# Optimization experiments

Hardware: AMD Instinct MI355X
Metric: run time of the kernel (lower is better)

The kernel has to match this reference:

```python
import jax, jax.numpy as jnp
import numpy as np
import math

B, L, E, H, FF = 8, 1024, 1024, 16, 4096
DH = E // H  # 64
EPS = 1e-10


def layer_norm(x, gamma, beta):
    mean = jnp.mean(x, axis=-1, keepdims=True)
    var = jnp.mean((x - mean) ** 2, axis=-1, keepdims=True)
    return gamma * (x - mean) / jnp.sqrt(var + EPS) + beta


def setup_inputs() -> dict:
    key = jax.random.key(0)
    ks = jax.random.split(key, 16)
    c_qk = math.sqrt(6.0 / (E + DH))
    c_o = math.sqrt(6.0 / (H * DH + E))
    c1 = math.sqrt(6.0 / (E + FF))
    c2 = math.sqrt(6.0 / (FF + E))
    u = lambda k, shp, c: jax.random.uniform(k, shp, jnp.float32, -c, c)
    return {
        "x": jax.random.normal(ks[0], (B, L, E), jnp.float32),
        # per-head projections stacked: [H, E, DH] (stored input-major = W^T of torch Linear)
        "Wq": u(ks[1], (H, E, DH), c_qk), "bq": jnp.zeros((H, DH), jnp.float32),
        "Wk": u(ks[2], (H, E, DH), c_qk), "bk": jnp.zeros((H, DH), jnp.float32),
        "Wv": u(ks[3], (H, E, DH), c_qk), "bv": jnp.zeros((H, DH), jnp.float32),
        "Wo": u(ks[4], (H * DH, E), c_o), "bo": jnp.zeros((E,), jnp.float32),
        "W1": u(ks[5], (E, FF), c1), "b1": jnp.zeros((FF,), jnp.float32),
        "W2": u(ks[6], (FF, E), c2), "b2": jnp.zeros((E,), jnp.float32),
        "gamma1": jnp.ones((E,), jnp.float32), "beta1": jnp.zeros((E,), jnp.float32),
        "gamma2": jnp.ones((E,), jnp.float32), "beta2": jnp.zeros((E,), jnp.float32),
    }


def reference(x, Wq, bq, Wk, bk, Wv, bv, Wo, bo, W1, b1, W2, b2, gamma1, beta1, gamma2, beta2):
    # multi-head attention (all heads batched; concat order == head order)
    q = jnp.einsum("ble,hed->bhld", x, Wq) + bq[None, :, None, :]
    k = jnp.einsum("ble,hed->bhld", x, Wk) + bk[None, :, None, :]
    v = jnp.einsum("ble,hed->bhld", x, Wv) + bv[None, :, None, :]
    scores = jnp.einsum("bhld,bhmd->bhlm", q, k) / math.sqrt(DH)
    weights = jax.nn.softmax(scores, axis=-1)
    y = jnp.einsum("bhlm,bhmd->bhld", weights, v)          # [B,H,L,DH]
    concat = y.transpose(0, 2, 1, 3).reshape(B, L, H * DH)  # [B,L,E]
    out1 = concat @ Wo + bo
    # residual + LN (dropout p=0 -> identity)
    out2 = layer_norm(out1 + x, gamma1, beta1)
    # FFN
    out3 = jax.nn.relu(out2 @ W1 + b1) @ W2 + b2
    return layer_norm(out3 + out2, gamma2, beta2)
```

## Files before the change

### kernel.cpp

```cpp
#include <hip/hip_runtime.h>
#include <hip/hip_bf16.h>

#define BB 8
#define LL 1024
#define EE 1024
#define HH 16
#define DHH 64
#define FFF 4096

typedef __attribute__((ext_vector_type(8))) short short8;
typedef __attribute__((ext_vector_type(4))) float f32x4;

__device__ inline f32x4 mfma16(short8 a, short8 b, f32x4 c) {
    return __builtin_amdgcn_mfma_f32_16x16x32_bf16(a, b, c, 0, 0, 0);
}

__device__ inline void async_ld16(const __hip_bfloat16* g, __hip_bfloat16* l) {
    __builtin_amdgcn_global_load_lds(
        (const __attribute__((address_space(1))) void*)g,
        (__attribute__((address_space(3))) void*)l, 16, 0, 0);
}

__device__ inline unsigned short bf16bits(float f) {
    __hip_bfloat16 h = __float2bfloat16(f);
    return *reinterpret_cast<unsigned short*>(&h);
}

__device__ inline float bf2f(unsigned short u) {
    unsigned v = ((unsigned)u) << 16;
    return *reinterpret_cast<float*>(&v);
}

__device__ inline float exp2_fast(float x) {
    float r;
    asm("v_exp_f32 %0, %1" : "=v"(r) : "v"(x));
    return r;
}

__device__ inline unsigned cvt_pk_bf16(float lo, float hi) {
    unsigned r;
    asm("v_cvt_pk_bf16_f32 %0, %1, %2" : "=v"(r) : "v"(lo), "v"(hi));
    return r;
}

__device__ inline void wg_barrier() {
    __builtin_amdgcn_sched_barrier(0);
    asm volatile("" ::: "memory");
    __builtin_amdgcn_s_barrier();
    asm volatile("" ::: "memory");
    __builtin_amdgcn_sched_barrier(0);
}

__global__ __launch_bounds__(256) void cvt_bf16(const float* __restrict__ in,
                                                __hip_bfloat16* __restrict__ out) {
    size_t i = (size_t)blockIdx.x * 256 + threadIdx.x;
    float4 v = reinterpret_cast<const float4*>(in)[i];
    ushort4 o;
    o.x = bf16bits(v.x); o.y = bf16bits(v.y); o.z = bf16bits(v.z); o.w = bf16bits(v.w);
    reinterpret_cast<ushort4*>(out)[i] = o;
}

__global__ __launch_bounds__(256) void wtrans_all(
    const float* __restrict__ Wq, const float* __restrict__ Wk, const float* __restrict__ Wv,
    const float* __restrict__ Wo, const float* __restrict__ W1, const float* __restrict__ W2,
    __hip_bfloat16* __restrict__ wqkvt, __hip_bfloat16* __restrict__ wot,
    __hip_bfloat16* __restrict__ w1t, __hip_bfloat16* __restrict__ w2t) {
    const int id = blockIdx.x;
    const float* src;
    __hip_bfloat16* dst;
    int K, N, k0, n0;
    if (id < 768) {
        const int which = id >> 8, r = id & 255;
        const int z = r >> 4, xx = r & 15;
        src = ((which == 0) ? Wq : (which == 1) ? Wk : Wv) + (size_t)z * 65536;
        dst = wqkvt + (size_t)which * 1024 * 1024 + (size_t)z * 65536;
        K = 1024; N = 64; k0 = xx * 64; n0 = 0;
    } else if (id < 1024) {
        const int r = id - 768;
        src = Wo; dst = wot; K = 1024; N = 1024; k0 = (r & 15) * 64; n0 = (r >> 4) * 64;
    } else if (id < 2048) {
        const int r = id - 1024;
        src = W1; dst = w1t; K = 1024; N = 4096; k0 = (r & 15) * 64; n0 = (r >> 4) * 64;
    } else {
        const int r = id - 2048;
        src = W2; dst = w2t; K = 4096; N = 1024; k0 = (r & 63) * 64; n0 = (r >> 6) * 64;
    }
    __shared__ __hip_bfloat16 t[64 * 66];
    const int tid = threadIdx.x;
#pragma unroll
    for (int i = 0; i < 16; ++i) {
        int idx = tid + i * 256;
        int kr = idx >> 6, nc = idx & 63;
        t[kr * 66 + nc] = __float2bfloat16(src[(size_t)(k0 + kr) * N + n0 + nc]);
    }
    __syncthreads();
#pragma unroll
    for (int i = 0; i < 16; ++i) {
        int idx = tid + i * 256;
        int nr = idx >> 6, kc = idx & 63;
        dst[(size_t)(n0 + nr) * K + k0 + kc] = t[kc * 66 + nr];
    }
}

__global__ __launch_bounds__(256) void vtrans(const __hip_bfloat16* __restrict__ qkv,
                                              __hip_bfloat16* __restrict__ vt) {
    const int bh = blockIdx.x, lt = blockIdx.y;
    const int b = bh >> 4, h = bh & 15;
    __shared__ __hip_bfloat16 t[64 * 66];
    const int tid = threadIdx.x;
#pragma unroll
    for (int i = 0; i < 16; ++i) {
        int idx = tid + i * 256;
        int lr = idx >> 6, d = idx & 63;
        t[lr * 66 + d] = qkv[(size_t)(b * LL + lt * 64 + lr) * 3072 + 2048 + h * 64 + d];
    }
    __syncthreads();
#pragma unroll
    for (int i = 0; i < 16; ++i) {
        int idx = tid + i * 256;
        int dr = idx >> 6, lc = idx & 63;
        vt[((size_t)bh * 64 + dr) * LL + lt * 64 + lc] = t[lc * 66 + dr];
    }
}

template <int MODE, int CM, int CN, int ZX>
__global__ __launch_bounds__(512, 2) void gemm256(
    const __hip_bfloat16* __restrict__ A, const __hip_bfloat16* __restrict__ Bm,
    int M, int N, int K, int ksplit, size_t zstride, void* __restrict__ Cout,
    const float* __restrict__ bias0, const float* __restrict__ bias1,
    const float* __restrict__ bias2) {
    __shared__ __hip_bfloat16 lds[2][2][2][128 * 64];
    const int flat = blockIdx.x + gridDim.x * (blockIdx.y + gridDim.y * blockIdx.z);
    const int xcd = flat & 7, rank = flat >> 3;
    const int mc = xcd & 3, hc = xcd >> 2;
    const int ml = rank / CN, nl = rank % CN;
    const int mb = mc * CM + ml;
    const int nb = ZX ? nl : (hc * CN + nl);
    const int zb = ZX ? hc : 0;
    const int m0 = mb * 256, n0 = nb * 256;
    const int tid = threadIdx.x;
    const int wid = tid >> 6, l = tid & 63;
    const int wm = wid >> 2, wn = wid & 3;
    const int lr = l & 15, lg = l >> 4;
    const int T = K / (64 * ksplit);
    const int kb = zb * T;

    const int c0 = tid, c1 = tid + 512;
    const int r0 = c0 >> 3, s0 = (((c0 & 7) ^ (r0 & 7)) << 3);
    const int r1 = c1 >> 3, s1 = (((c1 & 7) ^ (r1 & 7)) << 3);
    const int ldst0 = wid * 512;
    const int ldst1 = 4096 + wid * 512;

#define STAGE(bi, isb, half, kt)                                                             \
    do {                                                                                     \
        const __hip_bfloat16* _s = (isb) ? Bm : A;                                           \
        const int _br = ((isb) ? n0 : m0) + (half) * 128;                                    \
        __hip_bfloat16* _d = &lds[bi][isb][half][0];                                         \
        async_ld16(_s + (size_t)(_br + r0) * K + (size_t)(kb + (kt)) * 64 + s0, _d + ldst0); \
        async_ld16(_s + (size_t)(_br + r1) * K + (size_t)(kb + (kt)) * 64 + s1, _d + ldst1); \
    } while (0)

    f32x4 acc[8][4];
#pragma unroll
    for (int m = 0; m < 8; ++m)
#pragma unroll
        for (int n = 0; n < 4; ++n) acc[m][n] = (f32x4){0.f, 0.f, 0.f, 0.f};

    short8 aLo[4][2], aHi[4][2], bR[4][2];

#define LDA(dst, bi, m, kh)                                                          \
    do {                                                                             \
        const int _ra = (m) * 16 + lr;                                               \
        const int _sl = ((kh) * 4 + lg) ^ (_ra & 7);                                 \
        dst = *reinterpret_cast<const short8*>(&lds[bi][0][wm][_ra * 64 + _sl * 8]); \
    } while (0)
#define LDB(dst, bi, n, kh)                                                               \
    do {                                                                                  \
        const int _rb = (wn & 1) * 64 + (n) * 16 + lr;                                    \
        const int _sl = ((kh) * 4 + lg) ^ (_rb & 7);                                      \
        dst = *reinterpret_cast<const short8*>(&lds[bi][1][wn >> 1][_rb * 64 + _sl * 8]); \
    } while (0)

#define RD_ALO(bi)                      \
    _Pragma("unroll") for (int m = 0; m < 4; ++m) { \
        LDA(aLo[m][0], bi, m, 0);       \
        LDA(aLo[m][1], bi, m, 1);       \
    }
#define RD_AHI(bi)                      \
    _Pragma("unroll") for (int m = 0; m < 4; ++m) { \
        LDA(aHi[m][0], bi, m + 4, 0);   \
        LDA(aHi[m][1], bi, m + 4, 1);   \
    }
#define RD_B01(bi)                      \
    _Pragma("unroll") for (int n = 0; n < 2; ++n) { \
        LDB(bR[n][0], bi, n, 0);        \
        LDB(bR[n][1], bi, n, 1);        \
    }
#define RD_B23(bi)                      \
    _Pragma("unroll") for (int n = 2; n < 4; ++n) { \
        LDB(bR[n][0], bi, n, 0);        \
        LDB(bR[n][1], bi, n, 1);        \
    }
#define MFMA_Q(mbase, afr, nlo)                                            \
    __builtin_amdgcn_s_setprio(1);                                         \
    _Pragma("unroll") for (int m = 0; m < 4; ++m) {                        \
        _Pragma("unroll") for (int n = (nlo); n < (nlo) + 2; ++n) {        \
            acc[(mbase) + m][n] = mfma16(afr[m][0], bR[n][0], acc[(mbase) + m][n]); \
            acc[(mbase) + m][n] = mfma16(afr[m][1], bR[n][1], acc[(mbase) + m][n]); \
        }                                                                  \
    }                                                                      \
    __builtin_amdgcn_s_setprio(0);

    STAGE(0, 1, 0, 0);
    STAGE(0, 1, 1, 0);
    STAGE(0, 0, 0, 0);
    STAGE(0, 0, 1, 0);
    if (T > 1) {
        STAGE(1, 1, 0, 1);
        STAGE(1, 1, 1, 1);
        STAGE(1, 0, 0, 1);
        asm volatile("s_waitcnt vmcnt(6)" ::: "memory");
    } else {
        asm volatile("s_waitcnt vmcnt(0)" ::: "memory");
    }
    wg_barrier();
    RD_ALO(0);
    RD_B01(0);

    for (int t = 0; t < T; ++t) {
        const int cur = t & 1, nxt = cur ^ 1;
        wg_barrier();
        MFMA_Q(0, aLo, 0);
        RD_B23(cur);
        if (t + 1 < T) STAGE(nxt, 0, 1, t + 1);
        wg_barrier();
        MFMA_Q(0, aLo, 2);
        RD_AHI(cur);
        if (t + 2 < T) STAGE(cur, 1, 0, t + 2);
        wg_barrier();
        MFMA_Q(4, aHi, 0);
        if (t + 2 < T) {
            asm volatile("s_waitcnt vmcnt(2)" ::: "memory");
            STAGE(cur, 1, 1, t + 2);
            STAGE(cur, 0, 0, t + 2);
        } else if (t + 1 < T) {
            asm volatile("s_waitcnt vmcnt(0)" ::: "memory");
        }
        wg_barrier();
        MFMA_Q(4, aHi, 2);
        if (t + 1 < T) {
            RD_ALO(nxt);
            RD_B01(nxt);
        }
    }
#undef STAGE
#undef LDA
#undef LDB
#undef RD_ALO
#undef RD_AHI
#undef RD_B01
#undef RD_B23
#undef MFMA_Q

    asm volatile("s_waitcnt vmcnt(0)" ::: "memory");
    __syncthreads();

    float* eb = reinterpret_cast<float*>(&lds[0][0][0][0]) + wid * (16 * 68);
    const int erow = l >> 3, ec = l & 7;
    const int rowg = m0 + wm * 128;
    const int colg = n0 + wn * 64;
    float bv[4];
#pragma unroll
    for (int n = 0; n < 4; ++n) {
        if constexpr (MODE == 0) {
            const int col = colg + n * 16 + lr;
            int s = col >> 10;
            const float* bp = (s == 0) ? bias0 : ((s == 1) ? bias1 : bias2);
            bv[n] = bp[col & 1023];
        } else if constexpr (MODE == 2) {
            bv[n] = bias0[colg + n * 16 + lr];
        } else {
            bv[n] = 0.f;
        }
    }
    __hip_bfloat16* Cb = (MODE == 4)
        ? ((__hip_bfloat16*)Cout + (size_t)zb * zstride)
        : (__hip_bfloat16*)Cout;
#pragma unroll
    for (int m = 0; m < 8; ++m) {
#pragma unroll
        for (int n = 0; n < 4; ++n)
#pragma unroll
            for (int r = 0; r < 4; ++r) {
                float v = acc[m][n][r] + bv[n];
                if constexpr (MODE == 2) v = fmaxf(v, 0.f);
                eb[(lg * 4 + r) * 68 + n * 16 + lr] = v;
            }
#pragma unroll
        for (int i = 0; i < 2; ++i) {
            const int rr = erow + i * 8;
            float4 v0 = *reinterpret_cast<float4*>(&eb[rr * 68 + ec * 8]);
            float4 v1 = *reinterpret_cast<float4*>(&eb[rr * 68 + ec * 8 + 4]);
            uint4 o;
            o.x = cvt_pk_bf16(v0.x, v0.y);
            o.y = cvt_pk_bf16(v0.z, v0.w);
            o.z = cvt_pk_bf16(v1.x, v1.y);
            o.w = cvt_pk_bf16(v1.z, v1.w);
            *reinterpret_cast<uint4*>(&Cb[(size_t)(rowg + m * 16 + rr) * N + colg + ec * 8]) = o;
        }
    }
}

__global__ __launch_bounds__(512) void attn3(const __hip_bfloat16* __restrict__ qkv,
                                             const __hip_bfloat16* __restrict__ vt,
                                             __hip_bfloat16* __restrict__ cat) {
    const int orig = blockIdx.y * 8 + blockIdx.x;
    const int swz = (orig & 7) * 128 + (orig >> 3);
    const int qt = swz & 7, bh = swz >> 3;
    const int b = bh >> 4, h = bh & 15;
    const int tid = threadIdx.x, w = tid >> 6, l = tid & 63;
    const int lr = l & 15, lg = l >> 4;
    const int sw = lr & 7;

    __shared__ __hip_bfloat16 Ks[2][64 * 64];
    __shared__ __hip_bfloat16 Vs[2][64 * 64];
    __shared__ __hip_bfloat16 plds[8][16 * 72];

    const size_t qrow = (size_t)(b * LL + qt * 128 + w * 16 + lr);
    const short8 qa0 = *reinterpret_cast<const short8*>(qkv + qrow * 3072 + h * 64 + lg * 8);
    const short8 qa1 = *reinterpret_cast<const short8*>(qkv + qrow * 3072 + h * 64 + 32 + lg * 8);

    const int rA = tid >> 3, sA = (((tid & 7) ^ (rA & 7)) << 3);
    const __hip_bfloat16* kg = qkv + (size_t)(b * LL + rA) * 3072 + 1024 + h * 64 + sA;
    const __hip_bfloat16* vg = vt + ((size_t)bh * 64 + rA) * LL + sA;

#define STAGE_KV(bi, k0)                                        \
    do {                                                        \
        async_ld16(kg + (size_t)(k0) * 3072, &Ks[bi][w * 512]); \
        async_ld16(vg + (k0), &Vs[bi][w * 512]);                \
    } while (0)

    float mrun = -INFINITY, lrun = 0.f;
    f32x4 oacc[4];
#pragma unroll
    for (int n = 0; n < 4; ++n) oacc[n] = (f32x4){0.f, 0.f, 0.f, 0.f};

    STAGE_KV(0, 0);
    asm volatile("s_waitcnt vmcnt(0)" ::: "memory");
    __syncthreads();

    const float SCALE = 0.18033688011112042f;

    int cur = 0;
    for (int kt = 0; kt < 16; ++kt) {
        if (kt < 15) STAGE_KV(cur ^ 1, (kt + 1) * 64);

        f32x4 s[4];
#pragma unroll
        for (int m = 0; m < 4; ++m) {
            const int krow = m * 16 + lr;
            const short8 kf0 =
                *reinterpret_cast<const short8*>(&Ks[cur][krow * 64 + ((lg ^ sw) << 3)]);
            const short8 kf1 =
                *reinterpret_cast<const short8*>(&Ks[cur][krow * 64 + (((lg + 4) ^ sw) << 3)]);
            f32x4 t = (f32x4){0.f, 0.f, 0.f, 0.f};
            t = mfma16(kf0, qa0, t);
            t = mfma16(kf1, qa1, t);
            s[m] = t * SCALE;
        }
        float smax = s[0][0];
#pragma unroll
        for (int m = 0; m < 4; ++m)
#pragma unroll
            for (int r = 0; r < 4; ++r) smax = fmaxf(smax, s[m][r]);
        smax = fmaxf(smax, __shfl_xor(smax, 16, 64));
        smax = fmaxf(smax, __shfl_xor(smax, 32, 64));
        if (__any(smax > mrun + 8.0f)) {
            const float mnew = fmaxf(mrun, smax);
            const float alpha = exp2_fast(mrun - mnew);
            mrun = mnew;
            lrun *= alpha;
#pragma unroll
            for (int r = 0; r < 4; ++r) {
                const float aD = __shfl(alpha, lg * 4 + r, 64);
#pragma unroll
                for (int n = 0; n < 4; ++n) oacc[n][r] *= aD;
            }
        }
        float p[4][4];
        float tsum = 0.f;
#pragma unroll
        for (int m = 0; m < 4; ++m)
#pragma unroll
            for (int r = 0; r < 4; ++r) {
                p[m][r] = exp2_fast(s[m][r] - mrun);
                tsum += p[m][r];
            }
        tsum += __shfl_xor(tsum, 16, 64);
        tsum += __shfl_xor(tsum, 32, 64);
        lrun += tsum;

#pragma unroll
        for (int m = 0; m < 4; ++m) {
            uint2 d;
            d.x = cvt_pk_bf16(p[m][0], p[m][1]);
            d.y = cvt_pk_bf16(p[m][2], p[m][3]);
            *reinterpret_cast<uint2*>(&plds[w][lr * 72 + m * 16 + lg * 4]) = d;
        }
        asm volatile("s_waitcnt lgkmcnt(0)" ::: "memory");
        __builtin_amdgcn_sched_barrier(0);

        const short8 pa0 = *reinterpret_cast<const short8*>(&plds[w][lr * 72 + lg * 8]);
        const short8 pa1 = *reinterpret_cast<const short8*>(&plds[w][lr * 72 + 32 + lg * 8]);
#pragma unroll
        for (int n = 0; n < 4; ++n) {
            const int vrow = n * 16 + lr;
            const short8 vf0 =
                *reinterpret_cast<const short8*>(&Vs[cur][vrow * 64 + ((lg ^ sw) << 3)]);
            const short8 vf1 =
                *reinterpret_cast<const short8*>(&Vs[cur][vrow * 64 + (((lg + 4) ^ sw) << 3)]);
            oacc[n] = mfma16(pa0, vf0, oacc[n]);
            oacc[n] = mfma16(pa1, vf1, oacc[n]);
        }

        asm volatile("s_waitcnt vmcnt(0)" ::: "memory");
        __syncthreads();
        cur ^= 1;
    }
#undef STAGE_KV

    float rinv[4];
#pragma unroll
    for (int r = 0; r < 4; ++r) rinv[r] = 1.0f / __shfl(lrun, lg * 4 + r, 64);
#pragma unroll
    for (int n = 0; n < 4; ++n)
#pragma unroll
        for (int r = 0; r < 4; ++r) {
            const float v = oacc[n][r] * rinv[r];
            cat[(size_t)(b * LL + qt * 128 + w * 16 + lg * 4 + r) * EE + h * 64 + n * 16 + lr] =
                __float2bfloat16(v);
        }
}

template <bool CBF16, bool OUTF32>
__global__ __launch_bounds__(256) void ln_fused(const __hip_bfloat16* __restrict__ a,
                                                const __hip_bfloat16* __restrict__ b,
                                                const void* __restrict__ cv,
                                                const float* __restrict__ colbias,
                                                const float* __restrict__ gamma,
                                                const float* __restrict__ beta,
                                                void* __restrict__ outv) {
    const int row = blockIdx.x, tid = threadIdx.x;
    const size_t base = (size_t)row * EE;
    const ushort4 ua = reinterpret_cast<const ushort4*>(a + base)[tid];
    const ushort4 ub = reinterpret_cast<const ushort4*>(b + base)[tid];
    float4 z;
    if constexpr (CBF16) {
        const ushort4 uc =
            reinterpret_cast<const ushort4*>((const __hip_bfloat16*)cv + base)[tid];
        z.x = bf2f(uc.x); z.y = bf2f(uc.y); z.z = bf2f(uc.z); z.w = bf2f(uc.w);
    } else {
        z = reinterpret_cast<const float4*>((const float*)cv + base)[tid];
    }
    float4 cb = reinterpret_cast<const float4*>(colbias)[tid];
    float4 x;
    x.x = bf2f(ua.x) + bf2f(ub.x) + z.x + cb.x;
    x.y = bf2f(ua.y) + bf2f(ub.y) + z.y + cb.y;
    x.z = bf2f(ua.z) + bf2f(ub.z) + z.z + cb.z;
    x.w = bf2f(ua.w) + bf2f(ub.w) + z.w + cb.w;
    float s = x.x + x.y + x.z + x.w;
    float s2 = x.x * x.x + x.y * x.y + x.z * x.z + x.w * x.w;
#pragma unroll
    for (int msk = 1; msk < 64; msk <<= 1) {
        s += __shfl_xor(s, msk, 64);
        s2 += __shfl_xor(s2, msk, 64);
    }
    __shared__ float red[8];
    const int w = tid >> 6, l = tid & 63;
    if (l == 0) { red[w] = s; red[4 + w] = s2; }
    __syncthreads();
    s = red[0] + red[1] + red[2] + red[3];
    s2 = red[4] + red[5] + red[6] + red[7];
    const float mean = s * (1.f / 1024.f);
    const float var = s2 * (1.f / 1024.f) - mean * mean;
    const float rstd = rsqrtf(var + 1e-10f);
    float4 g = reinterpret_cast<const float4*>(gamma)[tid];
    float4 bt = reinterpret_cast<const float4*>(beta)[tid];
    float4 o;
    o.x = g.x * (x.x - mean) * rstd + bt.x;
    o.y = g.y * (x.y - mean) * rstd + bt.y;
    o.z = g.z * (x.z - mean) * rstd + bt.z;
    o.w = g.w * (x.w - mean) * rstd + bt.w;
    if constexpr (OUTF32) {
        reinterpret_cast<float4*>((float*)outv + base)[tid] = o;
    } else {
        ushort4 ob;
        ob.x = bf16bits(o.x); ob.y = bf16bits(o.y); ob.z = bf16bits(o.z); ob.w = bf16bits(o.w);
        reinterpret_cast<ushort4*>((__hip_bfloat16*)outv + base)[tid] = ob;
    }
}

extern "C" void kernel_launch(void* const* d_in, const int* in_sizes, int n_in,
                              void* d_out, int out_size, void* d_ws, size_t ws_size,
                              hipStream_t stream) {
    const float* x = (const float*)d_in[0];
    const float* Wq = (const float*)d_in[1];
    const float* bq = (const float*)d_in[2];
    const float* Wk = (const float*)d_in[3];
    const float* bk = (const float*)d_in[4];
    const float* Wv = (const float*)d_in[5];
    const float* bv = (const float*)d_in[6];
    const float* Wo = (const float*)d_in[7];
    const float* bo = (const float*)d_in[8];
    const float* W1 = (const float*)d_in[9];
    const float* b1 = (const float*)d_in[10];
    const float* W2 = (const float*)d_in[11];
    const float* b2 = (const float*)d_in[12];
    const float* gamma1 = (const float*)d_in[13];
    const float* beta1 = (const float*)d_in[14];
    const float* gamma2 = (const float*)d_in[15];
    const float* beta2 = (const float*)d_in[16];
    float* out = (float*)d_out;

    char* Wb = (char*)d_ws;
    const size_t MB = (size_t)1 << 20;
    if (ws_size < 168 * MB) return;
    __hip_bfloat16* xb = (__hip_bfloat16*)(Wb + 0 * MB);
    __hip_bfloat16* wqkvt = (__hip_bfloat16*)(Wb + 16 * MB);
    __hip_bfloat16* wot = (__hip_bfloat16*)(Wb + 22 * MB);
    __hip_bfloat16* w1t = (__hip_bfloat16*)(Wb + 24 * MB);
    __hip_bfloat16* w2t = (__hip_bfloat16*)(Wb + 32 * MB);
    __hip_bfloat16* qkvb = (__hip_bfloat16*)(Wb + 40 * MB);
    __hip_bfloat16* vtb = (__hip_bfloat16*)(Wb + 88 * MB);
    __hip_bfloat16* catb = (__hip_bfloat16*)(Wb + 104 * MB);
    __hip_bfloat16* p0 = (__hip_bfloat16*)(Wb + 40 * MB);
    __hip_bfloat16* out2b = (__hip_bfloat16*)(Wb + 136 * MB);
    __hip_bfloat16* hbuf = (__hip_bfloat16*)(Wb + 40 * MB);
    __hip_bfloat16* q0 = (__hip_bfloat16*)(Wb + 0 * MB);
    const size_t PSTRIDE = (size_t)8192 * 1024;

    cvt_bf16<<<8192, 256, 0, stream>>>(x, xb);
    wtrans_all<<<3072, 256, 0, stream>>>(Wq, Wk, Wv, Wo, W1, W2, wqkvt, wot, w1t, w2t);
    gemm256<0, 8, 6, 0><<<dim3(32, 12, 1), 512, 0, stream>>>(xb, wqkvt, 8192, 3072, 1024, 1, 0,
                                                             qkvb, bq, bk, bv);
    vtrans<<<dim3(128, 16), 256, 0, stream>>>(qkvb, vtb);
    attn3<<<dim3(8, 128), 512, 0, stream>>>(qkvb, vtb, catb);
    gemm256<4, 8, 4, 1><<<dim3(32, 4, 2), 512, 0, stream>>>(catb, wot, 8192, 1024, 1024, 2,
                                                            PSTRIDE, p0, nullptr, nullptr,
                                                            nullptr);
    ln_fused<false, false><<<8192, 256, 0, stream>>>(p0, p0 + PSTRIDE, x, bo, gamma1, beta1,
                                                     out2b);
    gemm256<2, 8, 8, 0><<<dim3(32, 16, 1), 512, 0, stream>>>(out2b, w1t, 8192, 4096, 1024, 1, 0,
                                                             hbuf, b1, nullptr, nullptr);
    gemm256<4, 8, 4, 1><<<dim3(32, 4, 2), 512, 0, stream>>>(hbuf, w2t, 8192, 1024, 4096, 2,
                                                            PSTRIDE, q0, nullptr, nullptr,
                                                            nullptr);
    ln_fused<true, true><<<8192, 256, 0, stream>>>(q0, q0 + PSTRIDE, out2b, b2, gamma2, beta2,
                                                   out);
}
```

Measured before the change: 308.1 us.

## Fuse x conversion, V transpose into QKV GEMM, and double attention rows per wave

```diff
diff --git a/kernel.cpp b/kernel.cpp
--- a/kernel.cpp
+++ b/kernel.cpp
@@ -51,21 +51,27 @@
     __builtin_amdgcn_sched_barrier(0);
 }
 
-__global__ __launch_bounds__(256) void cvt_bf16(const float* __restrict__ in,
-                                                __hip_bfloat16* __restrict__ out) {
-    size_t i = (size_t)blockIdx.x * 256 + threadIdx.x;
-    float4 v = reinterpret_cast<const float4*>(in)[i];
-    ushort4 o;
-    o.x = bf16bits(v.x); o.y = bf16bits(v.y); o.z = bf16bits(v.z); o.w = bf16bits(v.w);
-    reinterpret_cast<ushort4*>(out)[i] = o;
-}
-
 __global__ __launch_bounds__(256) void wtrans_all(
     const float* __restrict__ Wq, const float* __restrict__ Wk, const float* __restrict__ Wv,
     const float* __restrict__ Wo, const float* __restrict__ W1, const float* __restrict__ W2,
+    const float* __restrict__ x,
     __hip_bfloat16* __restrict__ wqkvt, __hip_bfloat16* __restrict__ wot,
-    __hip_bfloat16* __restrict__ w1t, __hip_bfloat16* __restrict__ w2t) {
+    __hip_bfloat16* __restrict__ w1t, __hip_bfloat16* __restrict__ w2t,
+    __hip_bfloat16* __restrict__ xb) {
     const int id = blockIdx.x;
+    const int tid = threadIdx.x;
+    if (id >= 3072) {
+        const int xi = id - 3072;
+#pragma unroll
+        for (int j = 0; j < 4; ++j) {
+            const size_t f4 = (size_t)xi * 1024 + j * 256 + tid;
+            float4 v = reinterpret_cast<const float4*>(x)[f4];
+            ushort4 o;
+            o.x = bf16bits(v.x); o.y = bf16bits(v.y); o.z = bf16bits(v.z); o.w = bf16bits(v.w);
+            reinterpret_cast<ushort4*>(xb)[f4] = o;
+        }
+        return;
+    }
     const float* src;
     __hip_bfloat16* dst;
     int K, N, k0, n0;
@@ -86,7 +92,6 @@
         src = W2; dst = w2t; K = 4096; N = 1024; k0 = (r & 63) * 64; n0 = (r >> 6) * 64;
     }
     __shared__ __hip_bfloat16 t[64 * 66];
-    const int tid = threadIdx.x;
 #pragma unroll
     for (int i = 0; i < 16; ++i) {
         int idx = tid + i * 256;
@@ -99,27 +104,6 @@
         int idx = tid + i * 256;
         int nr = idx >> 6, kc = idx & 63;
         dst[(size_t)(n0 + nr) * K + k0 + kc] = t[kc * 66 + nr];
-    }
-}
-
-__global__ __launch_bounds__(256) void vtrans(const __hip_bfloat16* __restrict__ qkv,
-                                              __hip_bfloat16* __restrict__ vt) {
-    const int bh = blockIdx.x, lt = blockIdx.y;
-    const int b = bh >> 4, h = bh & 15;
-    __shared__ __hip_bfloat16 t[64 * 66];
-    const int tid = threadIdx.x;
-#pragma unroll
-    for (int i = 0; i < 16; ++i) {
-        int idx = tid + i * 256;
-        int lr = idx >> 6, d = idx & 63;
-        t[lr * 66 + d] = qkv[(size_t)(b * LL + lt * 64 + lr) * 3072 + 2048 + h * 64 + d];
-    }
-    __syncthreads();
-#pragma unroll
-    for (int i = 0; i < 16; ++i) {
-        int idx = tid + i * 256;
-        int dr = idx >> 6, lc = idx & 63;
-        vt[((size_t)bh * 64 + dr) * LL + lt * 64 + lc] = t[lc * 66 + dr];
     }
 }
 
@@ -128,7 +112,7 @@
     const __hip_bfloat16* __restrict__ A, const __hip_bfloat16* __restrict__ Bm,
     int M, int N, int K, int ksplit, size_t zstride, void* __restrict__ Cout,
     const float* __restrict__ bias0, const float* __restrict__ bias1,
-    const float* __restrict__ bias2) {
+    const float* __restrict__ bias2, __hip_bfloat16* __restrict__ vtout) {
     __shared__ __hip_bfloat16 lds[2][2][2][128 * 64];
     const int flat = blockIdx.x + gridDim.x * (blockIdx.y + gridDim.y * blockIdx.z);
     const int xcd = flat & 7, rank = flat >> 3;
@@ -308,15 +292,34 @@
             o.w = cvt_pk_bf16(v1.z, v1.w);
             *reinterpret_cast<uint4*>(&Cb[(size_t)(rowg + m * 16 + rr) * N + colg + ec * 8]) = o;
         }
-    }
-}
-
-__global__ __launch_bounds__(512) void attn3(const __hip_bfloat16* __restrict__ qkv,
-                                             const __hip_bfloat16* __restrict__ vt,
-                                             __hip_bfloat16* __restrict__ cat) {
-    const int orig = blockIdx.y * 8 + blockIdx.x;
-    const int swz = (orig & 7) * 128 + (orig >> 3);
-    const int qt = swz & 7, bh = swz >> 3;
+        if constexpr (MODE == 0) {
+            if (colg >= 2048) {
+                const int h2 = (colg - 2048) >> 6;
+                const int bh2 = ((rowg >> 10) << 4) + h2;
+                const int l0 = (rowg & 1023) + m * 16;
+                uint4 o0, o1;
+                o0.x = cvt_pk_bf16(eb[0 * 68 + l], eb[1 * 68 + l]);
+                o0.y = cvt_pk_bf16(eb[2 * 68 + l], eb[3 * 68 + l]);
+                o0.z = cvt_pk_bf16(eb[4 * 68 + l], eb[5 * 68 + l]);
+                o0.w = cvt_pk_bf16(eb[6 * 68 + l], eb[7 * 68 + l]);
+                o1.x = cvt_pk_bf16(eb[8 * 68 + l], eb[9 * 68 + l]);
+                o1.y = cvt_pk_bf16(eb[10 * 68 + l], eb[11 * 68 + l]);
+                o1.z = cvt_pk_bf16(eb[12 * 68 + l], eb[13 * 68 + l]);
+                o1.w = cvt_pk_bf16(eb[14 * 68 + l], eb[15 * 68 + l]);
+                __hip_bfloat16* vrow = vtout + ((size_t)bh2 * 64 + l) * 1024 + l0;
+                *reinterpret_cast<uint4*>(vrow) = o0;
+                *reinterpret_cast<uint4*>(vrow + 8) = o1;
+            }
+        }
+    }
+}
+
+__global__ __launch_bounds__(512, 4) void attn4(const __hip_bfloat16* __restrict__ qkv,
+                                                const __hip_bfloat16* __restrict__ vt,
+                                                __hip_bfloat16* __restrict__ cat) {
+    const int orig = blockIdx.y * 4 + blockIdx.x;
+    const int swz = (orig & 7) * 64 + (orig >> 3);
+    const int qt = swz & 3, bh = swz >> 2;
     const int b = bh >> 4, h = bh & 15;
     const int tid = threadIdx.x, w = tid >> 6, l = tid & 63;
     const int lr = l & 15, lg = l >> 4;
@@ -324,11 +327,15 @@
 
     __shared__ __hip_bfloat16 Ks[2][64 * 64];
     __shared__ __hip_bfloat16 Vs[2][64 * 64];
-    __shared__ __hip_bfloat16 plds[8][16 * 72];
-
-    const size_t qrow = (size_t)(b * LL + qt * 128 + w * 16 + lr);
-    const short8 qa0 = *reinterpret_cast<const short8*>(qkv + qrow * 3072 + h * 64 + lg * 8);
-    const short8 qa1 = *reinterpret_cast<const short8*>(qkv + qrow * 3072 + h * 64 + 32 + lg * 8);
+    __shared__ __hip_bfloat16 plds[8][32 * 72];
+
+    short8 qa[2][2];
+#pragma unroll
+    for (int q = 0; q < 2; ++q) {
+        const size_t qrow = (size_t)(b * LL + qt * 256 + w * 32 + q * 16 + lr);
+        qa[q][0] = *reinterpret_cast<const short8*>(qkv + qrow * 3072 + h * 64 + lg * 8);
+        qa[q][1] = *reinterpret_cast<const short8*>(qkv + qrow * 3072 + h * 64 + 32 + lg * 8);
+    }
 
     const int rA = tid >> 3, sA = (((tid & 7) ^ (rA & 7)) << 3);
     const __hip_bfloat16* kg = qkv + (size_t)(b * LL + rA) * 3072 + 1024 + h * 64 + sA;
@@ -340,10 +347,12 @@
         async_ld16(vg + (k0), &Vs[bi][w * 512]);                \
     } while (0)
 
-    float mrun = -INFINITY, lrun = 0.f;
-    f32x4 oacc[4];
-#pragma unroll
-    for (int n = 0; n < 4; ++n) oacc[n] = (f32x4){0.f, 0.f, 0.f, 0.f};
+    float mrun[2] = {-INFINITY, -INFINITY}, lrun[2] = {0.f, 0.f};
+    f32x4 oacc[2][4];
+#pragma unroll
+    for (int q = 0; q < 2; ++q)
+#pragma unroll
+        for (int n = 0; n < 4; ++n) oacc[q][n] = (f32x4){0.f, 0.f, 0.f, 0.f};
 
     STAGE_KV(0, 0);
     asm volatile("s_waitcnt vmcnt(0)" ::: "memory");
@@ -355,7 +364,7 @@
     for (int kt = 0; kt < 16; ++kt) {
         if (kt < 15) STAGE_KV(cur ^ 1, (kt + 1) * 64);
 
-        f32x4 s[4];
+        f32x4 s[2][4];
 #pragma unroll
         for (int m = 0; m < 4; ++m) {
             const int krow = m * 16 + lr;
@@ -363,55 +372,70 @@
                 *reinterpret_cast<const short8*>(&Ks[cur][krow * 64 + ((lg ^ sw) << 3)]);
             const short8 kf1 =
                 *reinterpret_cast<const short8*>(&Ks[cur][krow * 64 + (((lg + 4) ^ sw) << 3)]);
-            f32x4 t = (f32x4){0.f, 0.f, 0.f, 0.f};
-            t = mfma16(kf0, qa0, t);
-            t = mfma16(kf1, qa1, t);
-            s[m] = t * SCALE;
-        }
-        float smax = s[0][0];
-#pragma unroll
-        for (int m = 0; m < 4; ++m)
-#pragma unroll
-            for (int r = 0; r < 4; ++r) smax = fmaxf(smax, s[m][r]);
-        smax = fmaxf(smax, __shfl_xor(smax, 16, 64));
-        smax = fmaxf(smax, __shfl_xor(smax, 32, 64));
-        if (__any(smax > mrun + 8.0f)) {
-            const float mnew = fmaxf(mrun, smax);
-            const float alpha = exp2_fast(mrun - mnew);
-            mrun = mnew;
-            lrun *= alpha;
-#pragma unroll
-            for (int r = 0; r < 4; ++r) {
-                const float aD = __shfl(alpha, lg * 4 + r, 64);
-#pragma unroll
-                for (int n = 0; n < 4; ++n) oacc[n][r] *= aD;
-            }
-        }
-        float p[4][4];
-        float tsum = 0.f;
-#pragma unroll
-        for (int m = 0; m < 4; ++m)
-#pragma unroll
-            for (int r = 0; r < 4; ++r) {
-                p[m][r] = exp2_fast(s[m][r] - mrun);
-                tsum += p[m][r];
-            }
-        tsum += __shfl_xor(tsum, 16, 64);
-        tsum += __shfl_xor(tsum, 32, 64);
-        lrun += tsum;
-
-#pragma unroll
-        for (int m = 0; m < 4; ++m) {
-            uint2 d;
-            d.x = cvt_pk_bf16(p[m][0], p[m][1]);
-            d.y = cvt_pk_bf16(p[m][2], p[m][3]);
-            *reinterpret_cast<uint2*>(&plds[w][lr * 72 + m * 16 + lg * 4]) = d;
+#pragma unroll
+            for (int q = 0; q < 2; ++q) {
+                f32x4 t = (f32x4){0.f, 0.f, 0.f, 0.f};
+                t = mfma16(kf0, qa[q][0], t);
+                t = mfma16(kf1, qa[q][1], t);
+                s[q][m] = t * SCALE;
+            }
+        }
+        float smax[2];
+#pragma unroll
+        for (int q = 0; q < 2; ++q) {
+            float mx = s[q][0][0];
+#pragma unroll
+            for (int m = 0; m < 4; ++m)
+#pragma unroll
+                for (int r = 0; r < 4; ++r) mx = fmaxf(mx, s[q][m][r]);
+            mx = fmaxf(mx, __shfl_xor(mx, 16, 64));
+            mx = fmaxf(mx, __shfl_xor(mx, 32, 64));
+            smax[q] = mx;
+        }
+        if (__any(fmaxf(smax[0] - mrun[0], smax[1] - mrun[1]) > 8.0f)) {
+#pragma unroll
+            for (int q = 0; q < 2; ++q) {
+                const float mnew = fmaxf(mrun[q], smax[q]);
+                const float alpha = exp2_fast(mrun[q] - mnew);
+                mrun[q] = mnew;
+                lrun[q] *= alpha;
+#pragma unroll
+                for (int r = 0; r < 4; ++r) {
+                    const float aD = __shfl(alpha, lg * 4 + r, 64);
+#pragma unroll
+                    for (int n = 0; n < 4; ++n) oacc[q][n][r] *= aD;
+                }
+            }
+        }
+#pragma unroll
+        for (int q = 0; q < 2; ++q) {
+            float tsum = 0.f;
+#pragma unroll
+            for (int m = 0; m < 4; ++m) {
+                float p0 = exp2_fast(s[q][m][0] - mrun[q]);
+                float p1 = exp2_fast(s[q][m][1] - mrun[q]);
+                float p2 = exp2_fast(s[q][m][2] - mrun[q]);
+                float p3 = exp2_fast(s[q][m][3] - mrun[q]);
+                tsum += (p0 + p1) + (p2 + p3);
+                uint2 d;
+                d.x = cvt_pk_bf16(p0, p1);
+                d.y = cvt_pk_bf16(p2, p3);
+                *reinterpret_cast<uint2*>(&plds[w][(q * 16 + lr) * 72 + m * 16 + lg * 4]) = d;
+            }
+            tsum += __shfl_xor(tsum, 16, 64);
+            tsum += __shfl_xor(tsum, 32, 64);
+            lrun[q] += tsum;
         }
         asm volatile("s_waitcnt lgkmcnt(0)" ::: "memory");
         __builtin_amdgcn_sched_barrier(0);
 
-        const short8 pa0 = *reinterpret_cast<const short8*>(&plds[w][lr * 72 + lg * 8]);
-        const short8 pa1 = *reinterpret_cast<const short8*>(&plds[w][lr * 72 + 32 + lg * 8]);
+        short8 pa[2][2];
+#pragma unroll
+        for (int q = 0; q < 2; ++q) {
+            pa[q][0] = *reinterpret_cast<const short8*>(&plds[w][(q * 16 + lr) * 72 + lg * 8]);
+            pa[q][1] =
+                *reinterpret_cast<const short8*>(&plds[w][(q * 16 + lr) * 72 + 32 + lg * 8]);
+        }
 #pragma unroll
         for (int n = 0; n < 4; ++n) {
             const int vrow = n * 16 + lr;
@@ -419,8 +443,11 @@
                 *reinterpret_cast<const short8*>(&Vs[cur][vrow * 64 + ((lg ^ sw) << 3)]);
             const short8 vf1 =
                 *reinterpret_cast<const short8*>(&Vs[cur][vrow * 64 + (((lg + 4) ^ sw) << 3)]);
-            oacc[n] = mfma16(pa0, vf0, oacc[n]);
-            oacc[n] = mfma16(pa1, vf1, oacc[n]);
+#pragma unroll
+            for (int q = 0; q < 2; ++q) {
+                oacc[q][n] = mfma16(pa[q][0], vf0, oacc[q][n]);
+                oacc[q][n] = mfma16(pa[q][1], vf1, oacc[q][n]);
+            }
         }
 
         asm volatile("s_waitcnt vmcnt(0)" ::: "memory");
@@ -429,17 +456,20 @@
     }
 #undef STAGE_KV
 
-    float rinv[4];
-#pragma unroll
-    for (int r = 0; r < 4; ++r) rinv[r] = 1.0f / __shfl(lrun, lg * 4 + r, 64);
-#pragma unroll
-    for (int n = 0; n < 4; ++n)
-#pragma unroll
-        for (int r = 0; r < 4; ++r) {
-            const float v = oacc[n][r] * rinv[r];
-            cat[(size_t)(b * LL + qt * 128 + w * 16 + lg * 4 + r) * EE + h * 64 + n * 16 + lr] =
-                __float2bfloat16(v);
-        }
+#pragma unroll
+    for (int q = 0; q < 2; ++q) {
+        float rinv[4];
+#pragma unroll
+        for (int r = 0; r < 4; ++r) rinv[r] = 1.0f / __shfl(lrun[q], lg * 4 + r, 64);
+#pragma unroll
+        for (int n = 0; n < 4; ++n)
+#pragma unroll
+            for (int r = 0; r < 4; ++r) {
+                const float v = oacc[q][n][r] * rinv[r];
+                cat[(size_t)(b * LL + qt * 256 + w * 32 + q * 16 + lg * 4 + r) * EE + h * 64 +
+                    n * 16 + lr] = __float2bfloat16(v);
+            }
+    }
 }
 
 template <bool CBF16, bool OUTF32>
@@ -539,22 +569,21 @@
     __hip_bfloat16* q0 = (__hip_bfloat16*)(Wb + 0 * MB);
     const size_t PSTRIDE = (size_t)8192 * 1024;
 
-    cvt_bf16<<<8192, 256, 0, stream>>>(x, xb);
-    wtrans_all<<<3072, 256, 0, stream>>>(Wq, Wk, Wv, Wo, W1, W2, wqkvt, wot, w1t, w2t);
+    wtrans_all<<<5120, 256, 0, stream>>>(Wq, Wk, Wv, Wo, W1, W2, x, wqkvt, wot, w1t, w2t, xb);
     gemm256<0, 8, 6, 0><<<dim3(32, 12, 1), 512, 0, stream>>>(xb, wqkvt, 8192, 3072, 1024, 1, 0,
-                                                             qkvb, bq, bk, bv);
-    vtrans<<<dim3(128, 16), 256, 0, stream>>>(qkvb, vtb);
-    attn3<<<dim3(8, 128), 512, 0, stream>>>(qkvb, vtb, catb);
+                                                             qkvb, bq, bk, bv, vtb);
+    attn4<<<dim3(4, 128), 512, 0, stream>>>(qkvb, vtb, catb);
     gemm256<4, 8, 4, 1><<<dim3(32, 4, 2), 512, 0, stream>>>(catb, wot, 8192, 1024, 1024, 2,
                                                             PSTRIDE, p0, nullptr, nullptr,
-                                                            nullptr);
+                                                            nullptr, nullptr);
     ln_fused<false, false><<<8192, 256, 0, stream>>>(p0, p0 + PSTRIDE, x, bo, gamma1, beta1,
                                                      out2b);
     gemm256<2, 8, 8, 0><<<dim3(32, 16, 1), 512, 0, stream>>>(out2b, w1t, 8192, 4096, 1024, 1, 0,
-                                                             hbuf, b1, nullptr, nullptr);
+                                                             hbuf, b1, nullptr, nullptr,
+                                                             nullptr);
     gemm256<4, 8, 4, 1><<<dim3(32, 4, 2), 512, 0, stream>>>(hbuf, w2t, 8192, 1024, 4096, 2,
                                                             PSTRIDE, q0, nullptr, nullptr,
-                                                            nullptr);
+                                                            nullptr, nullptr);
     ln_fused<true, true><<<8192, 256, 0, stream>>>(q0, q0 + PSTRIDE, out2b, b2, gamma2, beta2,
                                                    out);
 }
```

Result: faster. 299.6 us (-2.8%).
